# Kernel tuning notes

Hardware: AMD Instinct MI355X
Metric: run time of the kernel (lower is better)

Reference implementation:

```python
import jax, jax.numpy as jnp
import numpy as np


def _ohem_single(score, pos_mask, neg_mask):
    # score: [H,W] prob of negative class; masks: [H,W] bool
    n_pos = pos_mask.sum()
    n_neg = neg_mask.sum()
    k = jnp.minimum(3 * n_pos, n_neg)  # number of hard negatives to keep
    masked = jnp.where(neg_mask, score, jnp.inf).ravel()
    sorted_s = jnp.sort(masked)  # ascending; k lowest neg scores = hardest negatives
    thr = sorted_s[jnp.maximum(k - 1, 0)]
    sel = neg_mask & (score <= thr)
    use_all = (n_pos == 0) | (k == 0)
    return jnp.where(use_all, neg_mask, sel)


def _forward(target, logits):
    pixel_cls_labels = target[..., 0]              # [B,H,W]
    pixel_cls_weights = target[..., 1]             # [B,H,W]
    pixel_link_labels = target[..., 2:6]           # [B,H,W,4]
    pixel_link_weights = target[..., 6:10]         # [B,H,W,4]
    B, C, H, W = logits.shape
    num_neighbours = (C - 2) // 2
    pixel_cls_logits = logits[:, 0:2]              # [B,2,H,W]
    pixel_link_logits = logits[:, 2:]              # [B,2*nn,H,W]

    pos_mask = pixel_cls_labels > 0
    neg_mask = pixel_cls_labels == 0

    # per-pixel 2-class cross-entropy with label = pos_mask
    logp = jax.nn.log_softmax(pixel_cls_logits, axis=1)     # [B,2,H,W]
    labels = pos_mask.astype(jnp.int32)
    pixel_cls_loss = -jnp.take_along_axis(logp, labels[:, None], axis=1)[:, 0]  # [B,H,W]

    pixel_neg_scores = jax.nn.softmax(pixel_cls_logits, axis=1)[:, 0]  # [B,H,W]
    selected_neg = jax.vmap(_ohem_single)(pixel_neg_scores, pos_mask, neg_mask)
    selected_neg = selected_neg.astype(jnp.float32)

    n_pos = pos_mask.sum()
    n_neg = selected_neg.sum()
    w = pixel_cls_weights + selected_neg
    cls_loss = (pixel_cls_loss * w).sum() / (n_pos + n_neg)

    # link loss: 2-way CE per neighbour
    link_logits = pixel_link_logits.reshape(B, 2, num_neighbours, H, W)
    link_labels = jnp.transpose(pixel_link_labels, (0, 3, 1, 2)).astype(jnp.int32)  # [B,nn,H,W]
    logp_link = jax.nn.log_softmax(link_logits, axis=1)  # [B,2,nn,H,W]
    link_ce = -jnp.take_along_axis(logp_link, link_labels[:, None], axis=1)[:, 0]  # [B,nn,H,W]
    lw = jnp.transpose(pixel_link_weights, (0, 3, 1, 2))  # [B,nn,H,W]

    def get_loss(label):
        m = lw * (link_labels == label).astype(jnp.float32)
        return (link_ce * m).sum() / m.sum()

    neg_lambda = 1.0
    link_loss = get_loss(1) + neg_lambda * get_loss(0)
    link_loss = jnp.where(n_pos == 0, jnp.zeros_like(link_loss), link_loss)
    return cls_loss * 2, link_loss


def setup_inputs() -> dict:
    key = jax.random.key(0)
    k1, k2, k3, k4, k5 = jax.random.split(key, 5)
    B, H, W = 16, 256, 256
    cls_labels = jax.random.randint(k1, (B, H, W, 1), 0, 2).astype(jnp.float32)
    cls_weights = jax.random.uniform(k2, (B, H, W, 1))
    link_labels = jax.random.randint(k3, (B, H, W, 4), 0, 2).astype(jnp.float32)
    link_weights = jax.random.uniform(k4, (B, H, W, 4))
    target = jnp.concatenate([cls_labels, cls_weights, link_labels, link_weights], axis=-1)
    logits = jax.random.normal(k5, (B, 10, H, W), dtype=jnp.float32)
    return {"target": target, "logits": logits}


def reference(target, logits):
    return _forward(target, logits)
```

## Files before the change

### kernel.cpp

```cpp
#include <hip/hip_runtime.h>
#include <math.h>

#define BB   16
#define HW   65536
#define NPIX (BB * HW)
#define NT   256
#define PPT  2
#define NBLK (NPIX / (NT * PPT))
#define BPI  (NBLK / BB)

#define UARR_OFF  0ull
#define CLSL_OFF  (4ull << 20)
#define PART_OFF  (8ull << 20)
#define STATS_OFF ((8ull << 20) + (64ull << 10))
#define CTR_OFF   ((8ull << 20) + (128ull << 10))

#define S_NPOS    0
#define F_SELCNT  16
#define F_SELSUM  32
#define F_GLB     48

__device__ __forceinline__ unsigned fmap(float x) {
  unsigned b = __float_as_uint(x);
  return (b & 0x80000000u) ? ~b : (b | 0x80000000u);
}

__device__ __forceinline__ float softplus_neg_abs(float d) {
  return __logf(1.f + __expf(-fabsf(d)));
}

__device__ __forceinline__ void histSelect(unsigned* lhist, int nbins, unsigned k,
                                           unsigned* wt, unsigned* sh_bin,
                                           unsigned* sh_rank) {
  int lane = threadIdx.x & 63, wave = threadIdx.x >> 6;
  int per = nbins >> 8;
  unsigned s = 0;
  for (int j = 0; j < per; j++) s += lhist[threadIdx.x * per + j];
  unsigned x = s;
  for (int o = 1; o < 64; o <<= 1) { unsigned v = __shfl_up(x, o, 64); if (lane >= o) x += v; }
  if (lane == 63) wt[wave] = x;
  __syncthreads();
  unsigned woff = 0;
  for (int w = 0; w < wave; w++) woff += wt[w];
  unsigned incl = x + woff, excl = incl - s;
  if (excl < k && k <= incl) {
    unsigned cum = excl;
    for (int j = 0; j < per; j++) {
      unsigned c = lhist[threadIdx.x * per + j];
      if (k <= cum + c) { *sh_bin = (unsigned)(threadIdx.x * per + j); *sh_rank = k - cum; break; }
      cum += c;
    }
  }
  __syncthreads();
}

__global__ __launch_bounds__(NT, 4) void kA(
    const float* __restrict__ target, const float* __restrict__ logits,
    unsigned* __restrict__ uarr, float* __restrict__ clsl,
    float* __restrict__ part, unsigned* __restrict__ ctr) {
  __shared__ float4 sT4[NT * 5];
  __shared__ float red[8][4];
  if (blockIdx.x == 0 && threadIdx.x == 0) ctr[0] = 0u;

  const int P0 = blockIdx.x * (NT * PPT);
  const int p0 = P0 + threadIdx.x * PPT;
  const int b  = P0 >> 16;
  const int hw = p0 & 65535;
  const int lane = threadIdx.x & 63, wave = threadIdx.x >> 6;

  const float* lg = logits + (size_t)b * 10 * HW + hw;
  float2 L[10];
#pragma unroll
  for (int c = 0; c < 10; c++) L[c] = *(const float2*)(lg + (size_t)c * HW);

  const float4* tBase = (const float4*)(target + (size_t)P0 * 10);
  float4 T[5];
#pragma unroll
  for (int j = 0; j < 5; j++) T[j] = tBase[threadIdx.x + NT * j];
#pragma unroll
  for (int j = 0; j < 5; j++) sT4[threadIdx.x + NT * j] = T[j];
  __syncthreads();

  float tf[20];
#pragma unroll
  for (int m = 0; m < 5; m++) {
    float4 v = sT4[5 * threadIdx.x + m];
    tf[4 * m] = v.x; tf[4 * m + 1] = v.y; tf[4 * m + 2] = v.z; tf[4 * m + 3] = v.w;
  }

  float cpos = 0.f, cneg = 0.f, s1 = 0.f, m1 = 0.f, s0 = 0.f, m0 = 0.f, wcl = 0.f;
  float negsum = 0.f;
  float cl2[2];
  unsigned uu[2];
#pragma unroll
  for (int q = 0; q < PPT; q++) {
    float label = tf[10 * q];
    float wgt   = tf[10 * q + 1];
    bool pos = label > 0.f;
    bool neg = label == 0.f;
    float l0 = q ? L[0].y : L[0].x;
    float l1 = q ? L[1].y : L[1].x;
    float d = l0 - l1;
    float cl = fmaxf(l0, l1) + softplus_neg_abs(d) - (pos ? l1 : l0);
    cl2[q] = cl;
    wcl += cl * wgt;
    cpos += pos ? 1.f : 0.f;
    cneg += neg ? 1.f : 0.f;
    if (neg) negsum += cl;
    unsigned u = fmap(d);
    uu[q] = neg ? u : 0xFFFFFFFFu;
#pragma unroll
    for (int n = 0; n < 4; n++) {
      float a = q ? L[2 + n].y : L[2 + n].x;
      float c = q ? L[6 + n].y : L[6 + n].x;
      float ce0 = fmaxf(a, c) + softplus_neg_abs(a - c);
      int lab = (int)tf[10 * q + 2 + n];
      float ce = ce0 - (lab ? c : a);
      float w = tf[10 * q + 6 + n];
      if (lab) { m1 += w; s1 += w * ce; }
      else     { m0 += w; s0 += w * ce; }
    }
  }
  *(float2*)(clsl + p0) = make_float2(cl2[0], cl2[1]);
  *(uint2*)(uarr + p0)  = make_uint2(uu[0], uu[1]);

  float vals[8] = {cpos, cneg, s1, m1, s0, m0, wcl, negsum};
#pragma unroll
  for (int qq = 0; qq < 8; qq++) {
    float x = vals[qq];
    for (int o = 32; o; o >>= 1) x += __shfl_down(x, o, 64);
    if (lane == 0) red[qq][wave] = x;
  }
  __syncthreads();
  if (threadIdx.x < 8)
    part[(size_t)threadIdx.x * NBLK + blockIdx.x] =
        red[threadIdx.x][0] + red[threadIdx.x][1] + red[threadIdx.x][2] + red[threadIdx.x][3];
}

__global__ void kThresh(const unsigned* __restrict__ uarr, const float* __restrict__ clsl,
                        const float* __restrict__ part, unsigned* __restrict__ stats,
                        unsigned* __restrict__ ctr, float* __restrict__ out) {
  __shared__ unsigned lhist[4096];
  __shared__ unsigned wt[4];
  __shared__ unsigned shb, shr;
  __shared__ float shv[3];
  __shared__ float red2[5][4];
  __shared__ unsigned sh_t;
  const int img = blockIdx.x;
  const int lane = threadIdx.x & 63, wave = threadIdx.x >> 6;
  float* fstats = (float*)stats;

  if (threadIdx.x < 64) {
    int base = img * BPI + threadIdx.x;
    float cp = part[0 * NBLK + base] + part[0 * NBLK + base + 64];
    float cn = part[1 * NBLK + base] + part[1 * NBLK + base + 64];
    float ns = part[7 * NBLK + base] + part[7 * NBLK + base + 64];
    for (int o = 32; o; o >>= 1) {
      cp += __shfl_down(cp, o, 64);
      cn += __shfl_down(cn, o, 64);
      ns += __shfl_down(ns, o, 64);
    }
    if (threadIdx.x == 0) { shv[0] = cp; shv[1] = cn; shv[2] = ns; }
  }
  if (img == 0) {
#pragma unroll
    for (int s = 0; s < 5; s++) {
      const float* p = part + (size_t)(2 + s) * NBLK;
      float x = 0.f;
      for (int t = threadIdx.x; t < NBLK; t += NT) x += p[t];
      for (int o = 32; o; o >>= 1) x += __shfl_down(x, o, 64);
      if (lane == 0) red2[s][wave] = x;
    }
  }
  __syncthreads();
  if (img == 0 && threadIdx.x < 5)
    fstats[F_GLB + threadIdx.x] = red2[threadIdx.x][0] + red2[threadIdx.x][1] +
                                  red2[threadIdx.x][2] + red2[threadIdx.x][3];

  unsigned npos = (unsigned)(shv[0] + 0.5f);
  unsigned nneg = (unsigned)(shv[1] + 0.5f);
  float negsum = shv[2];
  if (threadIdx.x == 0) stats[S_NPOS + img] = npos;

  unsigned k = min(3u * npos, nneg);
  if (npos == 0u || k == 0u || k >= nneg) {
    if (threadIdx.x == 0) { fstats[F_SELCNT + img] = (float)nneg; fstats[F_SELSUM + img] = negsum; }
  } else {
    const uint4* u4 = (const uint4*)(uarr + (size_t)img * HW);
    for (int j = threadIdx.x; j < 4096; j += NT) lhist[j] = 0;
    __syncthreads();
    for (int j = threadIdx.x; j < HW / 4; j += NT) {
      uint4 v = u4[j];
      atomicAdd(&lhist[v.x >> 20], 1u);
      atomicAdd(&lhist[v.y >> 20], 1u);
      atomicAdd(&lhist[v.z >> 20], 1u);
      atomicAdd(&lhist[v.w >> 20], 1u);
    }
    __syncthreads();
    histSelect(lhist, 4096, k, wt, &shb, &shr);
    unsigned B1 = shb, r1 = shr;
    for (int j = threadIdx.x; j < 4096; j += NT) lhist[j] = 0;
    __syncthreads();
    for (int j = threadIdx.x; j < HW / 4; j += NT) {
      uint4 v = u4[j];
      if ((v.x >> 20) == B1) atomicAdd(&lhist[(v.x >> 8) & 0xFFFu], 1u);
      if ((v.y >> 20) == B1) atomicAdd(&lhist[(v.y >> 8) & 0xFFFu], 1u);
      if ((v.z >> 20) == B1) atomicAdd(&lhist[(v.z >> 8) & 0xFFFu], 1u);
      if ((v.w >> 20) == B1) atomicAdd(&lhist[(v.w >> 8) & 0xFFFu], 1u);
    }
    __syncthreads();
    histSelect(lhist, 4096, r1, wt, &shb, &shr);
    unsigned hi24 = (B1 << 12) | shb;
    unsigned r2 = shr;
    for (int j = threadIdx.x; j < 256; j += NT) lhist[j] = 0;
    __syncthreads();
    for (int j = threadIdx.x; j < HW / 4; j += NT) {
      uint4 v = u4[j];
      if ((v.x >> 8) == hi24) atomicAdd(&lhist[v.x & 0xFFu], 1u);
      if ((v.y >> 8) == hi24) atomicAdd(&lhist[v.y & 0xFFu], 1u);
      if ((v.z >> 8) == hi24) atomicAdd(&lhist[v.z & 0xFFu], 1u);
      if ((v.w >> 8) == hi24) atomicAdd(&lhist[v.w & 0xFFu], 1u);
    }
    __syncthreads();
    histSelect(lhist, 256, r2, wt, &shb, &shr);
    unsigned thr = (hi24 << 8) | shb;
    const float4* c4 = (const float4*)(clsl + (size_t)img * HW);
    float cnt = 0.f, sum = 0.f;
    for (int j = threadIdx.x; j < HW / 4; j += NT) {
      uint4 v = u4[j];
      float4 c = c4[j];
      if (v.x <= thr) { cnt += 1.f; sum += c.x; }
      if (v.y <= thr) { cnt += 1.f; sum += c.y; }
      if (v.z <= thr) { cnt += 1.f; sum += c.z; }
      if (v.w <= thr) { cnt += 1.f; sum += c.w; }
    }
    for (int o = 32; o; o >>= 1) { cnt += __shfl_down(cnt, o, 64); sum += __shfl_down(sum, o, 64); }
    if (lane == 0) { red2[0][wave] = cnt; red2[1][wave] = sum; }
    __syncthreads();
    if (threadIdx.x == 0) {
      fstats[F_SELCNT + img] = red2[0][0] + red2[0][1] + red2[0][2] + red2[0][3];
      fstats[F_SELSUM + img] = red2[1][0] + red2[1][1] + red2[1][2] + red2[1][3];
    }
  }

  __threadfence();
  __syncthreads();
  if (threadIdx.x == 0) sh_t = atomicAdd(&ctr[0], 1u);
  __syncthreads();
  if (sh_t != BB - 1) return;
  __threadfence();
  if (threadIdx.x == 0) {
    unsigned npos_t = 0;
    float nsel = 0.f, selsum = 0.f;
    for (int b = 0; b < BB; b++) {
      npos_t += stats[S_NPOS + b];
      nsel   += fstats[F_SELCNT + b];
      selsum += fstats[F_SELSUM + b];
    }
    float s1 = fstats[F_GLB + 0], m1 = fstats[F_GLB + 1];
    float s0 = fstats[F_GLB + 2], m0 = fstats[F_GLB + 3];
    float wcl = fstats[F_GLB + 4];
    out[0] = 2.f * (wcl + selsum) / ((float)npos_t + nsel);
    out[1] = (npos_t != 0u) ? (s1 / m1 + s0 / m0) : 0.f;
  }
}

extern "C" void kernel_launch(void* const* d_in, const int* in_sizes, int n_in,
                              void* d_out, int out_size, void* d_ws, size_t ws_size,
                              hipStream_t stream) {
  const float* target = (const float*)d_in[0];
  const float* logits = (const float*)d_in[1];
  float* out = (float*)d_out;
  char* ws = (char*)d_ws;

  unsigned* uarr  = (unsigned*)(ws + UARR_OFF);
  float*    clsl  = (float*)(ws + CLSL_OFF);
  float*    part  = (float*)(ws + PART_OFF);
  unsigned* stats = (unsigned*)(ws + STATS_OFF);
  unsigned* ctr   = (unsigned*)(ws + CTR_OFF);

  kA<<<NBLK, NT, 0, stream>>>(target, logits, uarr, clsl, part, ctr);
  kThresh<<<BB, NT, 0, stream>>>(uarr, clsl, part, stats, ctr, out);
}
```

Baseline: 115.8 us.

## Recompute selected-negative loss from sort keys and fold threshold stage into one block

Drops the per-pixel class-loss buffer written by the first kernel and instead rebuilds the negative-pixel loss from the stored order-preserving key of the logit difference. This removes 4 MB of writes and later reads. The threshold kernel becomes a single block that reduces all partials in shared memory and runs the radix select only for images that need it, one image after another, with no global atomic counter. The risk is that up to 16 images' three-pass histogram selects now run serially on one CU instead of in parallel across 16 blocks.

Measured after the change: 117.1 us. Within noise of the previous version (+1.1%).

```diff
diff --git a/kernel.cpp b/kernel.cpp
--- a/kernel.cpp
+++ b/kernel.cpp
@@ -10,15 +10,7 @@
 #define BPI  (NBLK / BB)
 
 #define UARR_OFF  0ull
-#define CLSL_OFF  (4ull << 20)
-#define PART_OFF  (8ull << 20)
-#define STATS_OFF ((8ull << 20) + (64ull << 10))
-#define CTR_OFF   ((8ull << 20) + (128ull << 10))
-
-#define S_NPOS    0
-#define F_SELCNT  16
-#define F_SELSUM  32
-#define F_GLB     48
+#define PART_OFF  (4ull << 20)
 
 __device__ __forceinline__ unsigned fmap(float x) {
   unsigned b = __float_as_uint(x);
@@ -27,6 +19,12 @@
 
 __device__ __forceinline__ float softplus_neg_abs(float d) {
   return __logf(1.f + __expf(-fabsf(d)));
+}
+
+__device__ __forceinline__ float cl_from_u(unsigned u) {
+  unsigned b = (u & 0x80000000u) ? (u & 0x7FFFFFFFu) : ~u;
+  float d = __uint_as_float(b);
+  return fmaxf(-d, 0.f) + softplus_neg_abs(d);
 }
 
 __device__ __forceinline__ void histSelect(unsigned* lhist, int nbins, unsigned k,
@@ -56,11 +54,9 @@
 
 __global__ __launch_bounds__(NT, 4) void kA(
     const float* __restrict__ target, const float* __restrict__ logits,
-    unsigned* __restrict__ uarr, float* __restrict__ clsl,
-    float* __restrict__ part, unsigned* __restrict__ ctr) {
+    unsigned* __restrict__ uarr, float* __restrict__ part) {
   __shared__ float4 sT4[NT * 5];
   __shared__ float red[8][4];
-  if (blockIdx.x == 0 && threadIdx.x == 0) ctr[0] = 0u;
 
   const int P0 = blockIdx.x * (NT * PPT);
   const int p0 = P0 + threadIdx.x * PPT;
@@ -90,7 +86,6 @@
 
   float cpos = 0.f, cneg = 0.f, s1 = 0.f, m1 = 0.f, s0 = 0.f, m0 = 0.f, wcl = 0.f;
   float negsum = 0.f;
-  float cl2[2];
   unsigned uu[2];
 #pragma unroll
   for (int q = 0; q < PPT; q++) {
@@ -102,7 +97,6 @@
     float l1 = q ? L[1].y : L[1].x;
     float d = l0 - l1;
     float cl = fmaxf(l0, l1) + softplus_neg_abs(d) - (pos ? l1 : l0);
-    cl2[q] = cl;
     wcl += cl * wgt;
     cpos += pos ? 1.f : 0.f;
     cneg += neg ? 1.f : 0.f;
@@ -121,8 +115,7 @@
       else     { m0 += w; s0 += w * ce; }
     }
   }
-  *(float2*)(clsl + p0) = make_float2(cl2[0], cl2[1]);
-  *(uint2*)(uarr + p0)  = make_uint2(uu[0], uu[1]);
+  *(uint2*)(uarr + p0) = make_uint2(uu[0], uu[1]);
 
   float vals[8] = {cpos, cneg, s1, m1, s0, m0, wcl, negsum};
 #pragma unroll
@@ -137,55 +130,70 @@
         red[threadIdx.x][0] + red[threadIdx.x][1] + red[threadIdx.x][2] + red[threadIdx.x][3];
 }
 
-__global__ void kThresh(const unsigned* __restrict__ uarr, const float* __restrict__ clsl,
-                        const float* __restrict__ part, unsigned* __restrict__ stats,
-                        unsigned* __restrict__ ctr, float* __restrict__ out) {
+__global__ void kThresh(const unsigned* __restrict__ uarr,
+                        const float* __restrict__ part,
+                        float* __restrict__ out) {
   __shared__ unsigned lhist[4096];
   __shared__ unsigned wt[4];
   __shared__ unsigned shb, shr;
-  __shared__ float shv[3];
   __shared__ float red2[5][4];
-  __shared__ unsigned sh_t;
-  const int img = blockIdx.x;
+  __shared__ float simg[3][16];
+  __shared__ float selcnt[16], selsum[16];
+  __shared__ float glb[5];
+  __shared__ unsigned needR;
   const int lane = threadIdx.x & 63, wave = threadIdx.x >> 6;
-  float* fstats = (float*)stats;
-
-  if (threadIdx.x < 64) {
-    int base = img * BPI + threadIdx.x;
-    float cp = part[0 * NBLK + base] + part[0 * NBLK + base + 64];
-    float cn = part[1 * NBLK + base] + part[1 * NBLK + base + 64];
-    float ns = part[7 * NBLK + base] + part[7 * NBLK + base + 64];
-    for (int o = 32; o; o >>= 1) {
-      cp += __shfl_down(cp, o, 64);
-      cn += __shfl_down(cn, o, 64);
-      ns += __shfl_down(ns, o, 64);
-    }
-    if (threadIdx.x == 0) { shv[0] = cp; shv[1] = cn; shv[2] = ns; }
-  }
-  if (img == 0) {
-#pragma unroll
-    for (int s = 0; s < 5; s++) {
-      const float* p = part + (size_t)(2 + s) * NBLK;
-      float x = 0.f;
-      for (int t = threadIdx.x; t < NBLK; t += NT) x += p[t];
-      for (int o = 32; o; o >>= 1) x += __shfl_down(x, o, 64);
-      if (lane == 0) red2[s][wave] = x;
-    }
-  }
-  __syncthreads();
-  if (img == 0 && threadIdx.x < 5)
-    fstats[F_GLB + threadIdx.x] = red2[threadIdx.x][0] + red2[threadIdx.x][1] +
-                                  red2[threadIdx.x][2] + red2[threadIdx.x][3];
-
-  unsigned npos = (unsigned)(shv[0] + 0.5f);
-  unsigned nneg = (unsigned)(shv[1] + 0.5f);
-  float negsum = shv[2];
-  if (threadIdx.x == 0) stats[S_NPOS + img] = npos;
-
-  unsigned k = min(3u * npos, nneg);
-  if (npos == 0u || k == 0u || k >= nneg) {
-    if (threadIdx.x == 0) { fstats[F_SELCNT + img] = (float)nneg; fstats[F_SELSUM + img] = negsum; }
-  } else {
+
+  if (threadIdx.x == 0) needR = 0u;
+
+  {
+    int img = threadIdx.x >> 4;
+    int tj  = threadIdx.x & 15;
+    float a0 = 0.f, a1 = 0.f, a7 = 0.f;
+#pragma unroll
+    for (int i = 0; i < BPI / 16; i++) {
+      int idx = img * BPI + tj + 16 * i;
+      a0 += part[0 * NBLK + idx];
+      a1 += part[1 * NBLK + idx];
+      a7 += part[7 * NBLK + idx];
+    }
+    for (int o = 8; o; o >>= 1) {
+      a0 += __shfl_down(a0, o, 16);
+      a1 += __shfl_down(a1, o, 16);
+      a7 += __shfl_down(a7, o, 16);
+    }
+    if (tj == 0) { simg[0][img] = a0; simg[1][img] = a1; simg[2][img] = a7; }
+  }
+#pragma unroll
+  for (int s = 0; s < 5; s++) {
+    const float* p = part + (size_t)(2 + s) * NBLK;
+    float x = 0.f;
+    for (int t = threadIdx.x; t < NBLK; t += NT) x += p[t];
+    for (int o = 32; o; o >>= 1) x += __shfl_down(x, o, 64);
+    if (lane == 0) red2[s][wave] = x;
+  }
+  __syncthreads();
+  if (threadIdx.x < 5)
+    glb[threadIdx.x] = red2[threadIdx.x][0] + red2[threadIdx.x][1] +
+                       red2[threadIdx.x][2] + red2[threadIdx.x][3];
+
+  if (threadIdx.x < BB) {
+    unsigned npos = (unsigned)(simg[0][threadIdx.x] + 0.5f);
+    unsigned nneg = (unsigned)(simg[1][threadIdx.x] + 0.5f);
+    unsigned k = min(3u * npos, nneg);
+    if (npos == 0u || k == 0u || k >= nneg) {
+      selcnt[threadIdx.x] = (float)nneg;
+      selsum[threadIdx.x] = simg[2][threadIdx.x];
+    } else {
+      atomicOr(&needR, 1u << threadIdx.x);
+    }
+  }
+  __syncthreads();
+
+  for (int img = 0; img < BB; img++) {
+    if (!(needR & (1u << img))) continue;
+    unsigned npos = (unsigned)(simg[0][img] + 0.5f);
+    unsigned nneg = (unsigned)(simg[1][img] + 0.5f);
+    unsigned k = min(3u * npos, nneg);
     const uint4* u4 = (const uint4*)(uarr + (size_t)img * HW);
     for (int j = threadIdx.x; j < 4096; j += NT) lhist[j] = 0;
     __syncthreads();
@@ -224,43 +232,34 @@
     __syncthreads();
     histSelect(lhist, 256, r2, wt, &shb, &shr);
     unsigned thr = (hi24 << 8) | shb;
-    const float4* c4 = (const float4*)(clsl + (size_t)img * HW);
     float cnt = 0.f, sum = 0.f;
     for (int j = threadIdx.x; j < HW / 4; j += NT) {
       uint4 v = u4[j];
-      float4 c = c4[j];
-      if (v.x <= thr) { cnt += 1.f; sum += c.x; }
-      if (v.y <= thr) { cnt += 1.f; sum += c.y; }
-      if (v.z <= thr) { cnt += 1.f; sum += c.z; }
-      if (v.w <= thr) { cnt += 1.f; sum += c.w; }
+      if (v.x <= thr) { cnt += 1.f; sum += cl_from_u(v.x); }
+      if (v.y <= thr) { cnt += 1.f; sum += cl_from_u(v.y); }
+      if (v.z <= thr) { cnt += 1.f; sum += cl_from_u(v.z); }
+      if (v.w <= thr) { cnt += 1.f; sum += cl_from_u(v.w); }
     }
     for (int o = 32; o; o >>= 1) { cnt += __shfl_down(cnt, o, 64); sum += __shfl_down(sum, o, 64); }
     if (lane == 0) { red2[0][wave] = cnt; red2[1][wave] = sum; }
     __syncthreads();
     if (threadIdx.x == 0) {
-      fstats[F_SELCNT + img] = red2[0][0] + red2[0][1] + red2[0][2] + red2[0][3];
-      fstats[F_SELSUM + img] = red2[1][0] + red2[1][1] + red2[1][2] + red2[1][3];
-    }
-  }
-
-  __threadfence();
-  __syncthreads();
-  if (threadIdx.x == 0) sh_t = atomicAdd(&ctr[0], 1u);
-  __syncthreads();
-  if (sh_t != BB - 1) return;
-  __threadfence();
+      selcnt[img] = red2[0][0] + red2[0][1] + red2[0][2] + red2[0][3];
+      selsum[img] = red2[1][0] + red2[1][1] + red2[1][2] + red2[1][3];
+    }
+    __syncthreads();
+  }
+
   if (threadIdx.x == 0) {
     unsigned npos_t = 0;
-    float nsel = 0.f, selsum = 0.f;
+    float nsel = 0.f, ssum = 0.f;
     for (int b = 0; b < BB; b++) {
-      npos_t += stats[S_NPOS + b];
-      nsel   += fstats[F_SELCNT + b];
-      selsum += fstats[F_SELSUM + b];
-    }
-    float s1 = fstats[F_GLB + 0], m1 = fstats[F_GLB + 1];
-    float s0 = fstats[F_GLB + 2], m0 = fstats[F_GLB + 3];
-    float wcl = fstats[F_GLB + 4];
-    out[0] = 2.f * (wcl + selsum) / ((float)npos_t + nsel);
+      npos_t += (unsigned)(simg[0][b] + 0.5f);
+      nsel   += selcnt[b];
+      ssum   += selsum[b];
+    }
+    float s1 = glb[0], m1 = glb[1], s0 = glb[2], m0 = glb[3], wcl = glb[4];
+    out[0] = 2.f * (wcl + ssum) / ((float)npos_t + nsel);
     out[1] = (npos_t != 0u) ? (s1 / m1 + s0 / m0) : 0.f;
   }
 }
@@ -273,12 +272,9 @@
   float* out = (float*)d_out;
   char* ws = (char*)d_ws;
 
-  unsigned* uarr  = (unsigned*)(ws + UARR_OFF);
-  float*    clsl  = (float*)(ws + CLSL_OFF);
-  float*    part  = (float*)(ws + PART_OFF);
-  unsigned* stats = (unsigned*)(ws + STATS_OFF);
-  unsigned* ctr   = (unsigned*)(ws + CTR_OFF);
-
-  kA<<<NBLK, NT, 0, stream>>>(target, logits, uarr, clsl, part, ctr);
-  kThresh<<<BB, NT, 0, stream>>>(uarr, clsl, part, stats, ctr, out);
-}
+  unsigned* uarr = (unsigned*)(ws + UARR_OFF);
+  float*    part = (float*)(ws + PART_OFF);
+
+  kA<<<NBLK, NT, 0, stream>>>(target, logits, uarr, part);
+  kThresh<<<1, NT, 0, stream>>>(uarr, part, out);
+}
```
